# Kernel optimization log

Measured on AMD Instinct MI355X. Metric: run time of the kernel, lower is better.

## Reference

```python
import jax, jax.numpy as jnp
import numpy as np
import math

B, S, H = 1, 2048, 4096
NH, HD = 32, 128  # heads, head_dim
ROPE_THETA = 10000.0
SINK = 4
RECENT_RATIO = 0.1


def setup_inputs() -> dict:
    key = jax.random.key(0)
    ks = jax.random.split(key, 5)
    scale = 0.02
    return {
        "hidden_states": jax.random.normal(ks[0], (B, S, H), jnp.float32),
        "Wq": jax.random.normal(ks[1], (H, H), jnp.float32) * scale,
        "Wk": jax.random.normal(ks[2], (H, H), jnp.float32) * scale,
        "Wv": jax.random.normal(ks[3], (H, H), jnp.float32) * scale,
        "Wo": jax.random.normal(ks[4], (H, H), jnp.float32) * scale,
        "position_ids": jnp.arange(S, dtype=jnp.int64)[None, :],
    }


def _rope(x, cos, sin):
    # x: [B, NH, S, HD]; rotate_half = cat(-x2, x1)
    half = x.shape[-1] // 2
    rot = jnp.concatenate([-x[..., half:], x[..., :half]], axis=-1)
    return x * cos + rot * sin


def reference(hidden_states, Wq, Wk, Wv, Wo, position_ids):
    b, s, h = hidden_states.shape
    # projections (torch Linear: x @ W^T), split heads -> [B, NH, S, HD]
    q = (hidden_states @ Wq.T).reshape(b, s, NH, HD).transpose(0, 2, 1, 3)
    k = (hidden_states @ Wk.T).reshape(b, s, NH, HD).transpose(0, 2, 1, 3)
    v = (hidden_states @ Wv.T).reshape(b, s, NH, HD).transpose(0, 2, 1, 3)

    # rotary embeddings from position_ids
    inv_freq = 1.0 / (ROPE_THETA ** (jnp.arange(0, HD, 2, dtype=jnp.float32) / HD))
    freqs = position_ids.astype(jnp.float32)[..., None] * inv_freq  # [B, S, HD/2]
    emb = jnp.concatenate([freqs, freqs], axis=-1)                   # [B, S, HD]
    cos = jnp.cos(emb)[:, None, :, :]
    sin = jnp.sin(emb)[:, None, :, :]
    q = _rope(q, cos, sin)
    k = _rope(k, cos, sin)

    # causal attention
    scores = jnp.einsum('bhqd,bhkd->bhqk', q, k) / math.sqrt(HD)
    neg = jnp.finfo(scores.dtype).min
    causal = jnp.tril(jnp.ones((s, s), dtype=bool))
    scores = jnp.where(causal[None, None], scores, neg)
    attn = jax.nn.softmax(scores, axis=-1)
    out = jnp.einsum('bhqk,bhkd->bhqd', attn, v)
    out = out.transpose(0, 2, 1, 3).reshape(b, s, h)
    attn_output = out @ Wo.T

    # H2O streaming cache eviction: sink (first 4) + recent window KV
    recent = int(s * RECENT_RATIO)
    k_evicted = jnp.concatenate([k[:, :, :SINK, :], k[:, :, s - recent:, :]], axis=2)
    v_evicted = jnp.concatenate([v[:, :, :SINK, :], v[:, :, s - recent:, :]], axis=2)
    return attn_output, k_evicted, v_evicted
```

## Files before the change

### kernel.cpp

```cpp
#include <hip/hip_runtime.h>
#include <hip/hip_bf16.h>

typedef __bf16 bf16;
typedef __bf16 bf16x4 __attribute__((ext_vector_type(4)));
typedef __bf16 bf16x8 __attribute__((ext_vector_type(8)));
typedef float f32x4 __attribute__((ext_vector_type(4)));

#define MFMA16(a, b, c) __builtin_amdgcn_mfma_f32_16x16x32_bf16(a, b, c, 0, 0, 0)

constexpr int S_LEN = 2048;
constexpr int HDIM = 4096;
constexpr int NHEADS = 32;
constexpr int HEADD = 128;
constexpr int SINKN = 4;
constexpr int RECENT = 204;
constexpr int EVROWS = SINKN + RECENT;
constexpr float QSCALE = 0.08838834764831845f;

constexpr int JOBS_PER_HEAD = 40;
constexpr int SLOTS_PER_HEAD = 36;
constexpr size_t SLOT_BYTES = 33792;

__device__ inline bf16x8 cvt8(const float* p) {
    float4 a = *(const float4*)p;
    float4 b = *(const float4*)(p + 4);
    return bf16x8{(bf16)a.x, (bf16)a.y, (bf16)a.z, (bf16)a.w,
                  (bf16)b.x, (bf16)b.y, (bf16)b.z, (bf16)b.w};
}

__device__ inline void gload16(const bf16* g, bf16* l) {
    __builtin_amdgcn_global_load_lds(
        (const __attribute__((address_space(1))) unsigned int*)g,
        (__attribute__((address_space(3))) unsigned int*)l, 16, 0, 0);
}

__global__ __launch_bounds__(256) void cvt_kernel(const float* __restrict__ in,
                                                  bf16* __restrict__ out, int n8) {
    int i = blockIdx.x * 256 + threadIdx.x;
    if (i >= n8) return;
    *(bf16x8*)(out + (size_t)i * 8) = cvt8(in + (size_t)i * 8);
}

__device__ __forceinline__ void stage_b256(const bf16* __restrict__ Bp, bf16* dst,
                                           int K, int kc, int tid) {
#pragma unroll
    for (int r = 0; r < 2; ++r) {
        int idx = r * 512 + tid;
        int row = idx >> 3;
        int gs = (idx & 7) ^ (row & 7);
        gload16(Bp + (size_t)row * K + kc + gs * 8, dst + idx * 8);
    }
}
template <int MH>
__device__ __forceinline__ void stage_a256(const bf16* __restrict__ Ap, bf16* dst,
                                           int K, int kc, int tid) {
#pragma unroll
    for (int r = 0; r < 2; ++r) {
        int idx = r * 512 + tid;
        int row = idx >> 3;
        int gs = (idx & 7) ^ (row & 7);
        gload16(Ap + (size_t)(MH * 128 + row) * K + kc + gs * 8,
                dst + MH * 8192 + idx * 8);
    }
}
template <int MH>
__device__ __forceinline__ void lda256(const bf16* buf, int wm, int lg, int lr,
                                       bf16x8 (&af)[2][2]) {
#pragma unroll
    for (int mt = 0; mt < 2; ++mt)
#pragma unroll
        for (int kk = 0; kk < 2; ++kk)
            af[mt][kk] = *(const bf16x8*)&buf[MH * 8192 + (wm * 32 + mt * 16 + lr) * 64 +
                                              (((kk * 4 + lg) ^ (lr & 7)) * 8)];
}
__device__ __forceinline__ void ldb256(const bf16* buf, int wn, int lg, int lr,
                                       bf16x8 (&bfr)[4][2]) {
#pragma unroll
    for (int nt = 0; nt < 4; ++nt)
#pragma unroll
        for (int kk = 0; kk < 2; ++kk)
            bfr[nt][kk] = *(const bf16x8*)&buf[(wn * 64 + nt * 16 + lr) * 64 +
                                               (((kk * 4 + lg) ^ (lr & 7)) * 8)];
}
template <int MH>
__device__ __forceinline__ void mma256(const bf16x8 (&af)[2][2], const bf16x8 (&bfr)[4][2],
                                       f32x4 (&acc)[2][2][4]) {
#pragma unroll
    for (int mt = 0; mt < 2; ++mt)
#pragma unroll
        for (int nt = 0; nt < 4; ++nt)
#pragma unroll
            for (int kk = 0; kk < 2; ++kk)
                acc[MH][mt][nt] = MFMA16(af[mt][kk], bfr[nt][kk], acc[MH][mt][nt]);
}

template <bool C_IS_F32>
__global__ __launch_bounds__(512, 2) void gemm256(const bf16* __restrict__ A,
                                                  const bf16* __restrict__ B,
                                                  void* __restrict__ Cv,
                                                  int M, int N, int K) {
    __shared__ bf16 Abuf[2][256 * 64];
    __shared__ bf16 Bbuf[2][128 * 64];

    const int tid = threadIdx.x;
    const int lane = tid & 63, wid = tid >> 6;
    const int wm = wid >> 1, wn = wid & 1;
    const int lg = lane >> 4, lr = lane & 15;

    const int bid = blockIdx.x;
    const int bx = (bid & 7) * 4 + (bid >> 6);
    const int by = (bid >> 3) & 7;
    const int m0 = by * 256, n0 = bx * 128;

    const bf16* Ap = A + (size_t)m0 * K;
    const bf16* Bp = B + (size_t)n0 * K;

    f32x4 acc[2][2][4] = {};
    bf16x8 af[2][2], bfr[4][2];

    stage_b256(Bp, Bbuf[0], K, 0, tid);
    stage_a256<0>(Ap, Abuf[0], K, 0, tid);
    stage_a256<1>(Ap, Abuf[0], K, 0, tid);
    asm volatile("s_waitcnt vmcnt(2)" ::: "memory");
    __builtin_amdgcn_s_barrier();

    const bf16 *Ard = Abuf[0], *Brd = Bbuf[0];
    bf16 *Awr = Abuf[1], *Bwr = Bbuf[1];

    const int NT = K / 64;
    for (int t = 0; t < NT - 1; ++t) {
        const int kc = (t + 1) * 64;
        ldb256(Brd, wn, lg, lr, bfr);
        lda256<0>(Ard, wm, lg, lr, af);
        stage_b256(Bp, Bwr, K, kc, tid);
        stage_a256<0>(Ap, Awr, K, kc, tid);
        __builtin_amdgcn_s_barrier();
        asm volatile("s_waitcnt lgkmcnt(0)" ::: "memory");
        __builtin_amdgcn_sched_barrier(0);
        __builtin_amdgcn_s_setprio(1);
        mma256<0>(af, bfr, acc);
        __builtin_amdgcn_s_setprio(0);
        asm volatile("s_waitcnt vmcnt(4)" ::: "memory");
        __builtin_amdgcn_s_barrier();
        lda256<1>(Ard, wm, lg, lr, af);
        stage_a256<1>(Ap, Awr, K, kc, tid);
        __builtin_amdgcn_s_barrier();
        asm volatile("s_waitcnt lgkmcnt(0)" ::: "memory");
        __builtin_amdgcn_sched_barrier(0);
        __builtin_amdgcn_s_setprio(1);
        mma256<1>(af, bfr, acc);
        __builtin_amdgcn_s_setprio(0);
        asm volatile("s_waitcnt vmcnt(2)" ::: "memory");
        __builtin_amdgcn_s_barrier();
        const bf16* tA = Ard; Ard = Awr; Awr = (bf16*)tA;
        const bf16* tB = Brd; Brd = Bwr; Bwr = (bf16*)tB;
    }
    asm volatile("s_waitcnt vmcnt(0)" ::: "memory");
    __builtin_amdgcn_s_barrier();
    ldb256(Brd, wn, lg, lr, bfr);
    lda256<0>(Ard, wm, lg, lr, af);
    mma256<0>(af, bfr, acc);
    lda256<1>(Ard, wm, lg, lr, af);
    mma256<1>(af, bfr, acc);

#pragma unroll
    for (int mh = 0; mh < 2; ++mh)
#pragma unroll
        for (int mt = 0; mt < 2; ++mt)
#pragma unroll
            for (int nt = 0; nt < 4; ++nt)
#pragma unroll
                for (int r = 0; r < 4; ++r) {
                    int row = m0 + mh * 128 + wm * 32 + mt * 16 + lg * 4 + r;
                    int col = n0 + wn * 64 + nt * 16 + lr;
                    if constexpr (C_IS_F32)
                        ((float*)Cv)[(size_t)row * N + col] = acc[mh][mt][nt][r];
                    else
                        ((bf16*)Cv)[(size_t)row * N + col] = (bf16)acc[mh][mt][nt][r];
                }
}

__global__ __launch_bounds__(256) void rope_kernel(bf16* __restrict__ q,
                                                   bf16* __restrict__ k) {
    const int s = blockIdx.x;
    const int t = threadIdx.x;
    const int hh = t >> 3;
    const int i0 = (t & 7) << 3;
    const size_t base = (size_t)s * HDIM + hh * HEADD;

    bf16x8 q1 = *(bf16x8*)(q + base + i0);
    bf16x8 q2 = *(bf16x8*)(q + base + 64 + i0);
    bf16x8 k1 = *(bf16x8*)(k + base + i0);
    bf16x8 k2 = *(bf16x8*)(k + base + 64 + i0);
    bf16x8 q1o, q2o, k1o, k2o;
    const float pos = (float)s;
#pragma unroll
    for (int j = 0; j < 8; ++j) {
        float f = pos * exp2f((float)(i0 + j) * (-0.2076205059304602f));
        float sn, cs;
        sincosf(f, &sn, &cs);
        float x1 = (float)q1[j], x2 = (float)q2[j];
        q1o[j] = (bf16)((x1 * cs - x2 * sn) * QSCALE);
        q2o[j] = (bf16)((x2 * cs + x1 * sn) * QSCALE);
        x1 = (float)k1[j]; x2 = (float)k2[j];
        k1o[j] = (bf16)(x1 * cs - x2 * sn);
        k2o[j] = (bf16)(x2 * cs + x1 * sn);
    }
    *(bf16x8*)(q + base + i0) = q1o;
    *(bf16x8*)(q + base + 64 + i0) = q2o;
    *(bf16x8*)(k + base + i0) = k1o;
    *(bf16x8*)(k + base + 64 + i0) = k2o;
}

__global__ __launch_bounds__(256) void transpose_v(const bf16* __restrict__ v,
                                                   bf16* __restrict__ vt) {
    __shared__ bf16 tile[64][136];
    const int h = blockIdx.x;
    const int s0 = blockIdx.y * 64;
    const int tid = threadIdx.x;
#pragma unroll
    for (int j = 0; j < 4; ++j) {
        int ch = tid + 256 * j;
        int row = ch >> 4, c8 = (ch & 15) << 3;
        *(bf16x8*)&tile[row][c8] =
            *(const bf16x8*)(v + (size_t)(s0 + row) * HDIM + h * HEADD + c8);
    }
    __syncthreads();
#pragma unroll
    for (int j = 0; j < 4; ++j) {
        int ch = tid + 256 * j;
        int d = ch >> 3, s8 = (ch & 7) << 3;
        bf16x8 w;
#pragma unroll
        for (int i = 0; i < 8; ++i) w[i] = tile[s8 + i][d];
        *(bf16x8*)(vt + ((size_t)h * HEADD + d) * S_LEN + s0 + s8) = w;
    }
}

__global__ __launch_bounds__(256, 2) void attn_kernel(const bf16* __restrict__ q,
                                                      const bf16* __restrict__ k,
                                                      const bf16* __restrict__ vt,
                                                      bf16* __restrict__ o,
                                                      char* __restrict__ partials) {
    __shared__ bf16 K_lds[2][64 * 128];
    __shared__ bf16 V_lds[128 * 64];
    __shared__ bf16 P_lds[4][32 * 72];

    const int tid = threadIdx.x;
    const int lane = tid & 63, wid = tid >> 6;
    const int lg = lane >> 4, lr = lane & 15;

    const int bj = blockIdx.x;
    const int h = bj / JOBS_PER_HEAD;
    const int within = JOBS_PER_HEAD - 1 - (bj % JOBS_PER_HEAD);
    int qb, chunk, nj;
    if (within < 4)       { qb = within; chunk = 0; nj = 1; }
    else if (within < 12) { int u2 = within - 4;  qb = 4  + (u2 >> 1); chunk = u2 & 1;        nj = 2; }
    else if (within < 24) { int u2 = within - 12; int q3 = u2 / 3; qb = 8 + q3; chunk = u2 - 3 * q3; nj = 3; }
    else                  { int u2 = within - 24; qb = 12 + (u2 >> 2); chunk = u2 & 3;        nj = 4; }
    const int q0 = qb * 128;
    const int ntiles = 2 * qb + 2;
    const int tb = chunk * 8;
    const int te = min(tb + 8, ntiles);

    bf16x8 aq[2][4];
#pragma unroll
    for (int rs = 0; rs < 2; ++rs)
#pragma unroll
        for (int dc = 0; dc < 4; ++dc)
            aq[rs][dc] = *(const bf16x8*)(q + (size_t)(q0 + wid * 32 + rs * 16 + lr) * HDIM +
                                          h * HEADD + dc * 32 + lg * 8);

    f32x4 oacc[2][8] = {};
    float m_[2] = {-1e30f, -1e30f};
    float l_[2] = {0.f, 0.f};
    bf16* pw = &P_lds[wid][0];

    {
        const int kv0 = tb << 6;
#pragma unroll
        for (int i = 0; i < 4; ++i) {
            const int c = wid * 4 + i;
            const int krow = 4 * c + (lane >> 4);
            const int kg = (lane & 15) ^ (krow & 7);
            gload16(k + (size_t)(kv0 + krow) * HDIM + h * HEADD + kg * 8,
                    &K_lds[0][c * 512]);
        }
    }

    int cur = 0;
    for (int t = tb; t < te; ++t) {
        const int kv0 = t << 6;
#pragma unroll
        for (int i = 0; i < 4; ++i) {
            const int c = wid * 4 + i;
            const int vrow = 8 * c + (lane >> 3);
            const int vg = (lane & 7) ^ (vrow & 7);
            gload16(vt + (size_t)(h * HEADD + vrow) * S_LEN + kv0 + vg * 8,
                    &V_lds[c * 512]);
        }
        if (t + 1 < te) {
            const int kvn = (t + 1) << 6;
#pragma unroll
            for (int i = 0; i < 4; ++i) {
                const int c = wid * 4 + i;
                const int krow = 4 * c + (lane >> 4);
                const int kg = (lane & 15) ^ (krow & 7);
                gload16(k + (size_t)(kvn + krow) * HDIM + h * HEADD + kg * 8,
                        &K_lds[cur ^ 1][c * 512]);
            }
            asm volatile("s_waitcnt vmcnt(8)" ::: "memory");
        } else {
            asm volatile("s_waitcnt vmcnt(4)" ::: "memory");
        }
        __builtin_amdgcn_s_barrier();
        __builtin_amdgcn_sched_barrier(0);

        const bf16* Kb = &K_lds[cur][0];
        f32x4 st[2][4] = {};
#pragma unroll
        for (int kt = 0; kt < 4; ++kt) {
            bf16x8 kf[4];
#pragma unroll
            for (int dc = 0; dc < 4; ++dc)
                kf[dc] = *(const bf16x8*)&Kb[(kt * 16 + lr) * 128 +
                                             (((dc * 4 + lg) ^ (lr & 7)) * 8)];
#pragma unroll
            for (int dc = 0; dc < 4; ++dc) {
                st[0][kt] = MFMA16(kf[dc], aq[0][dc], st[0][kt]);
                st[1][kt] = MFMA16(kf[dc], aq[1][dc], st[1][kt]);
            }
        }

#pragma unroll
        for (int rs = 0; rs < 2; ++rs) {
            const int qr0 = q0 + wid * 32 + rs * 16;
            const int qidx = qr0 + lr;
            const bool nm = (kv0 + 63) > qr0;
            float v[16];
#pragma unroll
            for (int kt = 0; kt < 4; ++kt)
#pragma unroll
                for (int r = 0; r < 4; ++r) {
                    float x = st[rs][kt][r];
                    if (nm && (kv0 + kt * 16 + lg * 4 + r > qidx)) x = -1e30f;
                    v[kt * 4 + r] = x;
                }
            float pm = v[0];
#pragma unroll
            for (int i = 1; i < 16; ++i) pm = fmaxf(pm, v[i]);
            pm = fmaxf(pm, __shfl_xor(pm, 16));
            pm = fmaxf(pm, __shfl_xor(pm, 32));

            if (__any(pm > m_[rs] + 8.0f)) {
                float mn = fmaxf(m_[rs], pm);
                float sc = __expf(m_[rs] - mn);
                m_[rs] = mn;
                l_[rs] *= sc;
                float scb[4];
#pragma unroll
                for (int r = 0; r < 4; ++r)
                    scb[r] = __uint_as_float(__builtin_amdgcn_ds_bpermute(
                        (lg * 4 + r) * 4, __float_as_uint(sc)));
#pragma unroll
                for (int dt = 0; dt < 8; ++dt)
#pragma unroll
                    for (int r = 0; r < 4; ++r) oacc[rs][dt][r] *= scb[r];
            }
            const float mn = m_[rs];
            float rsum = 0.f;
#pragma unroll
            for (int kt = 0; kt < 4; ++kt) {
                bf16x4 pk;
#pragma unroll
                for (int r = 0; r < 4; ++r) {
                    float p = __expf(v[kt * 4 + r] - mn);
                    rsum += p;
                    pk[r] = (bf16)p;
                }
                *(bf16x4*)&pw[(rs * 16 + lr) * 72 + kt * 16 + lg * 4] = pk;
            }
            rsum += __shfl_xor(rsum, 16);
            rsum += __shfl_xor(rsum, 32);
            l_[rs] += rsum;
        }

        if (t + 1 < te) asm volatile("s_waitcnt vmcnt(4)" ::: "memory");
        else            asm volatile("s_waitcnt vmcnt(0)" ::: "memory");
        __builtin_amdgcn_s_barrier();
        __builtin_amdgcn_sched_barrier(0);

        bf16x8 pa[2][2];
#pragma unroll
        for (int rs = 0; rs < 2; ++rs)
#pragma unroll
            for (int kt2 = 0; kt2 < 2; ++kt2)
                pa[rs][kt2] = *(const bf16x8*)&pw[(rs * 16 + lr) * 72 + kt2 * 32 + lg * 8];
#pragma unroll
        for (int kt2 = 0; kt2 < 2; ++kt2)
#pragma unroll
            for (int dt = 0; dt < 8; ++dt) {
                bf16x8 bv = *(const bf16x8*)&V_lds[(dt * 16 + lr) * 64 +
                                                   (((kt2 * 4 + lg) ^ (lr & 7)) * 8)];
                oacc[0][dt] = MFMA16(pa[0][kt2], bv, oacc[0][dt]);
                oacc[1][dt] = MFMA16(pa[1][kt2], bv, oacc[1][dt]);
            }

        __builtin_amdgcn_s_barrier();
        __builtin_amdgcn_sched_barrier(0);
        cur ^= 1;
    }

    if (nj == 1) {
#pragma unroll
        for (int rs = 0; rs < 2; ++rs) {
            float lb[4];
#pragma unroll
            for (int r = 0; r < 4; ++r)
                lb[r] = __uint_as_float(__builtin_amdgcn_ds_bpermute(
                    (lg * 4 + r) * 4, __float_as_uint(l_[rs])));
#pragma unroll
            for (int r = 0; r < 4; ++r) {
                float inv = 1.0f / lb[r];
                const int row = q0 + wid * 32 + rs * 16 + lg * 4 + r;
#pragma unroll
                for (int dt = 0; dt < 8; ++dt)
                    o[(size_t)row * HDIM + h * HEADD + dt * 16 + lr] =
                        (bf16)(oacc[rs][dt][r] * inv);
            }
        }
    } else {
        const int sb = (qb < 8) ? (qb - 4) * 2 : (qb < 12) ? 8 + (qb - 8) * 3
                                                           : 20 + (qb - 12) * 4;
        char* slotp = partials + ((size_t)h * SLOTS_PER_HEAD + sb + chunk) * SLOT_BYTES;
        bf16* Op = (bf16*)slotp;
        float* mp = (float*)(slotp + 32768);
        float* lp = mp + 128;
#pragma unroll
        for (int rs = 0; rs < 2; ++rs) {
            const int rowl = wid * 32 + rs * 16;
#pragma unroll
            for (int r = 0; r < 4; ++r)
#pragma unroll
                for (int dt = 0; dt < 8; ++dt)
                    Op[(rowl + lg * 4 + r) * HEADD + dt * 16 + lr] = (bf16)oacc[rs][dt][r];
            if (lg == 0) { mp[rowl + lr] = m_[rs]; lp[rowl + lr] = l_[rs]; }
        }
    }
}

__global__ __launch_bounds__(256) void combine_kernel(const char* __restrict__ partials,
                                                      bf16* __restrict__ o) {
    const int h = blockIdx.x;
    const int qb = 4 + blockIdx.y;
    const int nj = (2 * qb + 9) / 8;
    const int sb = (qb < 8) ? (qb - 4) * 2 : (qb < 12) ? 8 + (qb - 8) * 3
                                                       : 20 + (qb - 12) * 4;
    const char* base = partials + ((size_t)h * SLOTS_PER_HEAD + sb) * SLOT_BYTES;

    const int row = threadIdx.x >> 1;
    const int d0 = (threadIdx.x & 1) * 64;

    float mc[4], lc[4];
    float M = -1e30f;
    for (int c = 0; c < nj; ++c) {
        const char* sp = base + (size_t)c * SLOT_BYTES;
        mc[c] = ((const float*)(sp + 32768))[row];
        lc[c] = ((const float*)(sp + 33280))[row];
        M = fmaxf(M, mc[c]);
    }
    float denom = 0.f;
    float acc[64] = {};
    for (int c = 0; c < nj; ++c) {
        float wgt = __expf(mc[c] - M);
        denom += wgt * lc[c];
        const bf16* Op = (const bf16*)(base + (size_t)c * SLOT_BYTES);
#pragma unroll
        for (int j = 0; j < 8; ++j) {
            bf16x8 a = *(const bf16x8*)&Op[row * HEADD + d0 + j * 8];
#pragma unroll
            for (int e = 0; e < 8; ++e) acc[j * 8 + e] += wgt * (float)a[e];
        }
    }
    float inv = 1.0f / denom;
    bf16* dst = o + (size_t)(qb * 128 + row) * HDIM + h * HEADD + d0;
#pragma unroll
    for (int j = 0; j < 8; ++j) {
        bf16x8 w;
#pragma unroll
        for (int e = 0; e < 8; ++e) w[e] = (bf16)(acc[j * 8 + e] * inv);
        *(bf16x8*)&dst[j * 8] = w;
    }
}

__global__ __launch_bounds__(256) void evict_kernel(const bf16* __restrict__ k,
                                                    const bf16* __restrict__ v,
                                                    float* __restrict__ out) {
    const int total = NHEADS * EVROWS * HEADD;
    int idx = blockIdx.x * 256 + threadIdx.x;
    if (idx >= 2 * total) return;
    const int which = idx / total;
    const int rem = idx % total;
    const int hh = rem / (EVROWS * HEADD);
    const int i = (rem / HEADD) % EVROWS;
    const int d = rem % HEADD;
    const int s = (i < SINKN) ? i : (S_LEN - RECENT) + (i - SINKN);
    const bf16* src = which ? v : k;
    out[(size_t)S_LEN * HDIM + (size_t)which * total + rem] =
        (float)src[(size_t)s * HDIM + hh * HEADD + d];
}

extern "C" void kernel_launch(void* const* d_in, const int* in_sizes, int n_in,
                              void* d_out, int out_size, void* d_ws, size_t ws_size,
                              hipStream_t stream) {
    const float* hs = (const float*)d_in[0];
    const float* Wq = (const float*)d_in[1];
    const float* Wk = (const float*)d_in[2];
    const float* Wv = (const float*)d_in[3];
    const float* Wo = (const float*)d_in[4];
    float* out = (float*)d_out;

    const size_t MB = 1024 * 1024;
    char* w = (char*)d_ws;
    bf16* hs_bf = (bf16*)(w);
    bf16* W_bf  = (bf16*)(w + 16 * MB);
    char* part  = w;
    bf16* q_ws  = (bf16*)(w + 48 * MB);
    bf16* k_ws  = (bf16*)(w + 64 * MB);
    bf16* v_ws  = (bf16*)(w + 80 * MB);
    bf16* vt_ws = (bf16*)(w + 96 * MB);
    bf16* o_ws  = q_ws;

    const int nW8 = HDIM * HDIM / 8;
    const int nH8 = S_LEN * HDIM / 8;

    cvt_kernel<<<(nH8 + 255) / 256, 256, 0, stream>>>(hs, hs_bf, nH8);

    cvt_kernel<<<(nW8 + 255) / 256, 256, 0, stream>>>(Wq, W_bf, nW8);
    gemm256<false><<<256, 512, 0, stream>>>(hs_bf, W_bf, q_ws, S_LEN, HDIM, HDIM);
    cvt_kernel<<<(nW8 + 255) / 256, 256, 0, stream>>>(Wk, W_bf, nW8);
    gemm256<false><<<256, 512, 0, stream>>>(hs_bf, W_bf, k_ws, S_LEN, HDIM, HDIM);
    cvt_kernel<<<(nW8 + 255) / 256, 256, 0, stream>>>(Wv, W_bf, nW8);
    gemm256<false><<<256, 512, 0, stream>>>(hs_bf, W_bf, v_ws, S_LEN, HDIM, HDIM);

    rope_kernel<<<S_LEN, 256, 0, stream>>>(q_ws, k_ws);
    transpose_v<<<dim3(NHEADS, S_LEN / 64), 256, 0, stream>>>(v_ws, vt_ws);

    evict_kernel<<<(2 * NHEADS * EVROWS * HEADD + 255) / 256, 256, 0, stream>>>(k_ws, v_ws, out);

    attn_kernel<<<NHEADS * JOBS_PER_HEAD, 256, 0, stream>>>(q_ws, k_ws, vt_ws, o_ws, part);
    combine_kernel<<<dim3(NHEADS, 12), 256, 0, stream>>>(part, o_ws);

    cvt_kernel<<<(nW8 + 255) / 256, 256, 0, stream>>>(Wo, W_bf, nW8);
    gemm256<true><<<256, 512, 0, stream>>>(o_ws, W_bf, out, S_LEN, HDIM, HDIM);
}
```

Before: 443.5 us.

## Fuse fp32-to-bf16 weight conversion into GEMM B-operand staging

Removes the four standalone weight conversion kernels and has each GEMM load fp32 weight tiles into registers, convert them to bf16, and write them into swizzled LDS itself. This avoids writing and re-reading a 32MB bf16 copy of each weight matrix and saves four launches. In exchange, B tiles now pass through registers instead of direct global-to-LDS loads, each block reads twice the bytes for B, and the pipeline's waitcnt and barrier placement changes, which may expose more load latency.

```diff
diff --git a/kernel.cpp b/kernel.cpp
--- a/kernel.cpp
+++ b/kernel.cpp
@@ -28,6 +28,11 @@
                   (bf16)b.x, (bf16)b.y, (bf16)b.z, (bf16)b.w};
 }
 
+__device__ __forceinline__ bf16x8 cvt8f(const float4& a, const float4& b) {
+    return bf16x8{(bf16)a.x, (bf16)a.y, (bf16)a.z, (bf16)a.w,
+                  (bf16)b.x, (bf16)b.y, (bf16)b.z, (bf16)b.w};
+}
+
 __device__ inline void gload16(const bf16* g, bf16* l) {
     __builtin_amdgcn_global_load_lds(
         (const __attribute__((address_space(1))) unsigned int*)g,
@@ -41,16 +46,6 @@
     *(bf16x8*)(out + (size_t)i * 8) = cvt8(in + (size_t)i * 8);
 }
 
-__device__ __forceinline__ void stage_b256(const bf16* __restrict__ Bp, bf16* dst,
-                                           int K, int kc, int tid) {
-#pragma unroll
-    for (int r = 0; r < 2; ++r) {
-        int idx = r * 512 + tid;
-        int row = idx >> 3;
-        int gs = (idx & 7) ^ (row & 7);
-        gload16(Bp + (size_t)row * K + kc + gs * 8, dst + idx * 8);
-    }
-}
 template <int MH>
 __device__ __forceinline__ void stage_a256(const bf16* __restrict__ Ap, bf16* dst,
                                            int K, int kc, int tid) {
@@ -63,6 +58,20 @@
                 dst + MH * 8192 + idx * 8);
     }
 }
+__device__ __forceinline__ void loadB_f32(const float* __restrict__ Bp, int K, int kc,
+                                          int tid, float4 (&br)[4]) {
+    const float* p = Bp + (size_t)(tid >> 2) * K + kc + (tid & 3) * 16;
+    br[0] = *(const float4*)p;
+    br[1] = *(const float4*)(p + 4);
+    br[2] = *(const float4*)(p + 8);
+    br[3] = *(const float4*)(p + 12);
+}
+__device__ __forceinline__ void writeB_lds(bf16* dst, int tid, const float4 (&br)[4]) {
+    const int row = tid >> 2;
+    const int c8 = (tid & 3) * 2;
+    *(bf16x8*)&dst[row * 64 + ((c8 ^ (row & 7)) * 8)] = cvt8f(br[0], br[1]);
+    *(bf16x8*)&dst[row * 64 + (((c8 + 1) ^ (row & 7)) * 8)] = cvt8f(br[2], br[3]);
+}
 template <int MH>
 __device__ __forceinline__ void lda256(const bf16* buf, int wm, int lg, int lr,
                                        bf16x8 (&af)[2][2]) {
@@ -96,7 +105,7 @@
 
 template <bool C_IS_F32>
 __global__ __launch_bounds__(512, 2) void gemm256(const bf16* __restrict__ A,
-                                                  const bf16* __restrict__ B,
+                                                  const float* __restrict__ B,
                                                   void* __restrict__ Cv,
                                                   int M, int N, int K) {
     __shared__ bf16 Abuf[2][256 * 64];
@@ -113,15 +122,20 @@
     const int m0 = by * 256, n0 = bx * 128;
 
     const bf16* Ap = A + (size_t)m0 * K;
-    const bf16* Bp = B + (size_t)n0 * K;
+    const float* Bp = B + (size_t)n0 * K;
 
     f32x4 acc[2][2][4] = {};
     bf16x8 af[2][2], bfr[4][2];
-
-    stage_b256(Bp, Bbuf[0], K, 0, tid);
+    float4 br[4];
+
+    loadB_f32(Bp, K, 0, tid, br);
+    __builtin_amdgcn_sched_barrier(0);
     stage_a256<0>(Ap, Abuf[0], K, 0, tid);
     stage_a256<1>(Ap, Abuf[0], K, 0, tid);
-    asm volatile("s_waitcnt vmcnt(2)" ::: "memory");
+    __builtin_amdgcn_sched_barrier(0);
+    asm volatile("s_waitcnt vmcnt(4)" ::: "memory");
+    writeB_lds(Bbuf[0], tid, br);
+    asm volatile("s_waitcnt vmcnt(0) lgkmcnt(0)" ::: "memory");
     __builtin_amdgcn_s_barrier();
 
     const bf16 *Ard = Abuf[0], *Brd = Bbuf[0];
@@ -132,7 +146,8 @@
         const int kc = (t + 1) * 64;
         ldb256(Brd, wn, lg, lr, bfr);
         lda256<0>(Ard, wm, lg, lr, af);
-        stage_b256(Bp, Bwr, K, kc, tid);
+        loadB_f32(Bp, K, kc, tid, br);
+        __builtin_amdgcn_sched_barrier(0);
         stage_a256<0>(Ap, Awr, K, kc, tid);
         __builtin_amdgcn_s_barrier();
         asm volatile("s_waitcnt lgkmcnt(0)" ::: "memory");
@@ -140,27 +155,29 @@
         __builtin_amdgcn_s_setprio(1);
         mma256<0>(af, bfr, acc);
         __builtin_amdgcn_s_setprio(0);
-        asm volatile("s_waitcnt vmcnt(4)" ::: "memory");
-        __builtin_amdgcn_s_barrier();
         lda256<1>(Ard, wm, lg, lr, af);
         stage_a256<1>(Ap, Awr, K, kc, tid);
-        __builtin_amdgcn_s_barrier();
+        __builtin_amdgcn_sched_barrier(0);
+        asm volatile("s_waitcnt vmcnt(4)" ::: "memory");
+        writeB_lds(Bwr, tid, br);
         asm volatile("s_waitcnt lgkmcnt(0)" ::: "memory");
         __builtin_amdgcn_sched_barrier(0);
         __builtin_amdgcn_s_setprio(1);
         mma256<1>(af, bfr, acc);
         __builtin_amdgcn_s_setprio(0);
-        asm volatile("s_waitcnt vmcnt(2)" ::: "memory");
+        asm volatile("s_waitcnt vmcnt(0)" ::: "memory");
         __builtin_amdgcn_s_barrier();
         const bf16* tA = Ard; Ard = Awr; Awr = (bf16*)tA;
         const bf16* tB = Brd; Brd = Bwr; Bwr = (bf16*)tB;
     }
-    asm volatile("s_waitcnt vmcnt(0)" ::: "memory");
-    __builtin_amdgcn_s_barrier();
     ldb256(Brd, wn, lg, lr, bfr);
     lda256<0>(Ard, wm, lg, lr, af);
+    asm volatile("s_waitcnt lgkmcnt(0)" ::: "memory");
+    __builtin_amdgcn_sched_barrier(0);
     mma256<0>(af, bfr, acc);
     lda256<1>(Ard, wm, lg, lr, af);
+    asm volatile("s_waitcnt lgkmcnt(0)" ::: "memory");
+    __builtin_amdgcn_sched_barrier(0);
     mma256<1>(af, bfr, acc);
 
 #pragma unroll
@@ -523,7 +540,6 @@
     const size_t MB = 1024 * 1024;
     char* w = (char*)d_ws;
     bf16* hs_bf = (bf16*)(w);
-    bf16* W_bf  = (bf16*)(w + 16 * MB);
     char* part  = w;
     bf16* q_ws  = (bf16*)(w + 48 * MB);
     bf16* k_ws  = (bf16*)(w + 64 * MB);
@@ -531,17 +547,13 @@
     bf16* vt_ws = (bf16*)(w + 96 * MB);
     bf16* o_ws  = q_ws;
 
-    const int nW8 = HDIM * HDIM / 8;
     const int nH8 = S_LEN * HDIM / 8;
 
     cvt_kernel<<<(nH8 + 255) / 256, 256, 0, stream>>>(hs, hs_bf, nH8);
 
-    cvt_kernel<<<(nW8 + 255) / 256, 256, 0, stream>>>(Wq, W_bf, nW8);
-    gemm256<false><<<256, 512, 0, stream>>>(hs_bf, W_bf, q_ws, S_LEN, HDIM, HDIM);
-    cvt_kernel<<<(nW8 + 255) / 256, 256, 0, stream>>>(Wk, W_bf, nW8);
-    gemm256<false><<<256, 512, 0, stream>>>(hs_bf, W_bf, k_ws, S_LEN, HDIM, HDIM);
-    cvt_kernel<<<(nW8 + 255) / 256, 256, 0, stream>>>(Wv, W_bf, nW8);
-    gemm256<false><<<256, 512, 0, stream>>>(hs_bf, W_bf, v_ws, S_LEN, HDIM, HDIM);
+    gemm256<false><<<256, 512, 0, stream>>>(hs_bf, Wq, q_ws, S_LEN, HDIM, HDIM);
+    gemm256<false><<<256, 512, 0, stream>>>(hs_bf, Wk, k_ws, S_LEN, HDIM, HDIM);
+    gemm256<false><<<256, 512, 0, stream>>>(hs_bf, Wv, v_ws, S_LEN, HDIM, HDIM);
 
     rope_kernel<<<S_LEN, 256, 0, stream>>>(q_ws, k_ws);
     transpose_v<<<dim3(NHEADS, S_LEN / 64), 256, 0, stream>>>(v_ws, vt_ws);
@@ -551,6 +563,5 @@
     attn_kernel<<<NHEADS * JOBS_PER_HEAD, 256, 0, stream>>>(q_ws, k_ws, vt_ws, o_ws, part);
     combine_kernel<<<dim3(NHEADS, 12), 256, 0, stream>>>(part, o_ws);
 
-    cvt_kernel<<<(nW8 + 255) / 256, 256, 0, stream>>>(Wo, W_bf, nW8);
-    gemm256<true><<<256, 512, 0, stream>>>(o_ws, W_bf, out, S_LEN, HDIM, HDIM);
-}
+    gemm256<true><<<256, 512, 0, stream>>>(o_ws, Wo, out, S_LEN, HDIM, HDIM);
+}
```

Result: slower. 639.3 us (+44.1%).

## Shrink projection GEMM tiles to 128x128 and simplify the double-buffer pipeline

Applied to the files above, without the earlier changes.

The projection GEMMs now use 128x128 output tiles instead of 256x128 and launch 512 blocks instead of 256. Launch bounds are raised to allow 4 blocks per CU with half the A-tile shared memory. The split two-half MFMA pipeline becomes a simpler loop: stage the next tile, wait, then load fragments and compute. This aims to fill more CUs and raise occupancy, at the cost of less data reuse per tile and more global/L2 traffic.

```diff
diff --git a/kernel.cpp b/kernel.cpp
--- a/kernel.cpp
+++ b/kernel.cpp
@@ -41,39 +41,35 @@
     *(bf16x8*)(out + (size_t)i * 8) = cvt8(in + (size_t)i * 8);
 }
 
-__device__ __forceinline__ void stage_b256(const bf16* __restrict__ Bp, bf16* dst,
-                                           int K, int kc, int tid) {
+__device__ __forceinline__ void stage128(const bf16* __restrict__ Ap,
+                                         const bf16* __restrict__ Bp,
+                                         bf16* Adst, bf16* Bdst,
+                                         int K, int kc, int tid) {
 #pragma unroll
     for (int r = 0; r < 2; ++r) {
         int idx = r * 512 + tid;
         int row = idx >> 3;
         int gs = (idx & 7) ^ (row & 7);
-        gload16(Bp + (size_t)row * K + kc + gs * 8, dst + idx * 8);
-    }
-}
-template <int MH>
-__device__ __forceinline__ void stage_a256(const bf16* __restrict__ Ap, bf16* dst,
-                                           int K, int kc, int tid) {
+        gload16(Ap + (size_t)row * K + kc + gs * 8, Adst + idx * 8);
+    }
 #pragma unroll
     for (int r = 0; r < 2; ++r) {
         int idx = r * 512 + tid;
         int row = idx >> 3;
         int gs = (idx & 7) ^ (row & 7);
-        gload16(Ap + (size_t)(MH * 128 + row) * K + kc + gs * 8,
-                dst + MH * 8192 + idx * 8);
-    }
-}
-template <int MH>
-__device__ __forceinline__ void lda256(const bf16* buf, int wm, int lg, int lr,
+        gload16(Bp + (size_t)row * K + kc + gs * 8, Bdst + idx * 8);
+    }
+}
+__device__ __forceinline__ void lda128(const bf16* buf, int wm, int lg, int lr,
                                        bf16x8 (&af)[2][2]) {
 #pragma unroll
     for (int mt = 0; mt < 2; ++mt)
 #pragma unroll
         for (int kk = 0; kk < 2; ++kk)
-            af[mt][kk] = *(const bf16x8*)&buf[MH * 8192 + (wm * 32 + mt * 16 + lr) * 64 +
+            af[mt][kk] = *(const bf16x8*)&buf[(wm * 32 + mt * 16 + lr) * 64 +
                                               (((kk * 4 + lg) ^ (lr & 7)) * 8)];
 }
-__device__ __forceinline__ void ldb256(const bf16* buf, int wn, int lg, int lr,
+__device__ __forceinline__ void ldb128(const bf16* buf, int wn, int lg, int lr,
                                        bf16x8 (&bfr)[4][2]) {
 #pragma unroll
     for (int nt = 0; nt < 4; ++nt)
@@ -82,24 +78,13 @@
             bfr[nt][kk] = *(const bf16x8*)&buf[(wn * 64 + nt * 16 + lr) * 64 +
                                                (((kk * 4 + lg) ^ (lr & 7)) * 8)];
 }
-template <int MH>
-__device__ __forceinline__ void mma256(const bf16x8 (&af)[2][2], const bf16x8 (&bfr)[4][2],
-                                       f32x4 (&acc)[2][2][4]) {
-#pragma unroll
-    for (int mt = 0; mt < 2; ++mt)
-#pragma unroll
-        for (int nt = 0; nt < 4; ++nt)
-#pragma unroll
-            for (int kk = 0; kk < 2; ++kk)
-                acc[MH][mt][nt] = MFMA16(af[mt][kk], bfr[nt][kk], acc[MH][mt][nt]);
-}
 
 template <bool C_IS_F32>
-__global__ __launch_bounds__(512, 2) void gemm256(const bf16* __restrict__ A,
+__global__ __launch_bounds__(512, 4) void gemm128(const bf16* __restrict__ A,
                                                   const bf16* __restrict__ B,
                                                   void* __restrict__ Cv,
                                                   int M, int N, int K) {
-    __shared__ bf16 Abuf[2][256 * 64];
+    __shared__ bf16 Abuf[2][128 * 64];
     __shared__ bf16 Bbuf[2][128 * 64];
 
     const int tid = threadIdx.x;
@@ -108,76 +93,70 @@
     const int lg = lane >> 4, lr = lane & 15;
 
     const int bid = blockIdx.x;
-    const int bx = (bid & 7) * 4 + (bid >> 6);
-    const int by = (bid >> 3) & 7;
-    const int m0 = by * 256, n0 = bx * 128;
+    const int xcd = bid & 7, wi = bid >> 3;
+    const int bx = xcd * 4 + (wi >> 4);
+    const int by = wi & 15;
+    const int m0 = by * 128, n0 = bx * 128;
 
     const bf16* Ap = A + (size_t)m0 * K;
     const bf16* Bp = B + (size_t)n0 * K;
 
-    f32x4 acc[2][2][4] = {};
+    f32x4 acc[2][4] = {};
     bf16x8 af[2][2], bfr[4][2];
 
-    stage_b256(Bp, Bbuf[0], K, 0, tid);
-    stage_a256<0>(Ap, Abuf[0], K, 0, tid);
-    stage_a256<1>(Ap, Abuf[0], K, 0, tid);
-    asm volatile("s_waitcnt vmcnt(2)" ::: "memory");
-    __builtin_amdgcn_s_barrier();
-
-    const bf16 *Ard = Abuf[0], *Brd = Bbuf[0];
-    bf16 *Awr = Abuf[1], *Bwr = Bbuf[1];
-
+    stage128(Ap, Bp, Abuf[0], Bbuf[0], K, 0, tid);
+
+    int cur = 0;
     const int NT = K / 64;
     for (int t = 0; t < NT - 1; ++t) {
-        const int kc = (t + 1) * 64;
-        ldb256(Brd, wn, lg, lr, bfr);
-        lda256<0>(Ard, wm, lg, lr, af);
-        stage_b256(Bp, Bwr, K, kc, tid);
-        stage_a256<0>(Ap, Awr, K, kc, tid);
+        stage128(Ap, Bp, Abuf[cur ^ 1], Bbuf[cur ^ 1], K, (t + 1) * 64, tid);
+        asm volatile("s_waitcnt vmcnt(4)" ::: "memory");
         __builtin_amdgcn_s_barrier();
+        __builtin_amdgcn_sched_barrier(0);
+
+        lda128(Abuf[cur], wm, lg, lr, af);
+        ldb128(Bbuf[cur], wn, lg, lr, bfr);
         asm volatile("s_waitcnt lgkmcnt(0)" ::: "memory");
         __builtin_amdgcn_sched_barrier(0);
         __builtin_amdgcn_s_setprio(1);
-        mma256<0>(af, bfr, acc);
+#pragma unroll
+        for (int mt = 0; mt < 2; ++mt)
+#pragma unroll
+            for (int nt = 0; nt < 4; ++nt)
+#pragma unroll
+                for (int kk = 0; kk < 2; ++kk)
+                    acc[mt][nt] = MFMA16(af[mt][kk], bfr[nt][kk], acc[mt][nt]);
         __builtin_amdgcn_s_setprio(0);
-        asm volatile("s_waitcnt vmcnt(4)" ::: "memory");
         __builtin_amdgcn_s_barrier();
-        lda256<1>(Ard, wm, lg, lr, af);
-        stage_a256<1>(Ap, Awr, K, kc, tid);
-        __builtin_amdgcn_s_barrier();
-        asm volatile("s_waitcnt lgkmcnt(0)" ::: "memory");
-        __builtin_amdgcn_sched_barrier(0);
-        __builtin_amdgcn_s_setprio(1);
-        mma256<1>(af, bfr, acc);
-        __builtin_amdgcn_s_setprio(0);
-        asm volatile("s_waitcnt vmcnt(2)" ::: "memory");
-        __builtin_amdgcn_s_barrier();
-        const bf16* tA = Ard; Ard = Awr; Awr = (bf16*)tA;
-        const bf16* tB = Brd; Brd = Bwr; Bwr = (bf16*)tB;
+        cur ^= 1;
     }
     asm volatile("s_waitcnt vmcnt(0)" ::: "memory");
     __builtin_amdgcn_s_barrier();
-    ldb256(Brd, wn, lg, lr, bfr);
-    lda256<0>(Ard, wm, lg, lr, af);
-    mma256<0>(af, bfr, acc);
-    lda256<1>(Ard, wm, lg, lr, af);
-    mma256<1>(af, bfr, acc);
-
-#pragma unroll
-    for (int mh = 0; mh < 2; ++mh)
-#pragma unroll
-        for (int mt = 0; mt < 2; ++mt)
-#pragma unroll
-            for (int nt = 0; nt < 4; ++nt)
-#pragma unroll
-                for (int r = 0; r < 4; ++r) {
-                    int row = m0 + mh * 128 + wm * 32 + mt * 16 + lg * 4 + r;
-                    int col = n0 + wn * 64 + nt * 16 + lr;
-                    if constexpr (C_IS_F32)
-                        ((float*)Cv)[(size_t)row * N + col] = acc[mh][mt][nt][r];
-                    else
-                        ((bf16*)Cv)[(size_t)row * N + col] = (bf16)acc[mh][mt][nt][r];
-                }
+    lda128(Abuf[cur], wm, lg, lr, af);
+    ldb128(Bbuf[cur], wn, lg, lr, bfr);
+    asm volatile("s_waitcnt lgkmcnt(0)" ::: "memory");
+    __builtin_amdgcn_sched_barrier(0);
+#pragma unroll
+    for (int mt = 0; mt < 2; ++mt)
+#pragma unroll
+        for (int nt = 0; nt < 4; ++nt)
+#pragma unroll
+            for (int kk = 0; kk < 2; ++kk)
+                acc[mt][nt] = MFMA16(af[mt][kk], bfr[nt][kk], acc[mt][nt]);
+
+#pragma unroll
+    for (int mt = 0; mt < 2; ++mt)
+#pragma unroll
+        for (int nt = 0; nt < 4; ++nt)
+#pragma unroll
+            for (int r = 0; r < 4; ++r) {
+                int row = m0 + wm * 32 + mt * 16 + lg * 4 + r;
+                int col = n0 + wn * 64 + nt * 16 + lr;
+                if constexpr (C_IS_F32)
+                    ((float*)Cv)[(size_t)row * N + col] = acc[mt][nt][r];
+                else
+                    ((bf16*)Cv)[(size_t)row * N + col] = (bf16)acc[mt][nt][r];
+            }
 }
 
 __global__ __launch_bounds__(256) void rope_kernel(bf16* __restrict__ q,
@@ -537,11 +516,11 @@
     cvt_kernel<<<(nH8 + 255) / 256, 256, 0, stream>>>(hs, hs_bf, nH8);
 
     cvt_kernel<<<(nW8 + 255) / 256, 256, 0, stream>>>(Wq, W_bf, nW8);
-    gemm256<false><<<256, 512, 0, stream>>>(hs_bf, W_bf, q_ws, S_LEN, HDIM, HDIM);
+    gemm128<false><<<512, 512, 0, stream>>>(hs_bf, W_bf, q_ws, S_LEN, HDIM, HDIM);
     cvt_kernel<<<(nW8 + 255) / 256, 256, 0, stream>>>(Wk, W_bf, nW8);
-    gemm256<false><<<256, 512, 0, stream>>>(hs_bf, W_bf, k_ws, S_LEN, HDIM, HDIM);
+    gemm128<false><<<512, 512, 0, stream>>>(hs_bf, W_bf, k_ws, S_LEN, HDIM, HDIM);
     cvt_kernel<<<(nW8 + 255) / 256, 256, 0, stream>>>(Wv, W_bf, nW8);
-    gemm256<false><<<256, 512, 0, stream>>>(hs_bf, W_bf, v_ws, S_LEN, HDIM, HDIM);
+    gemm128<false><<<512, 512, 0, stream>>>(hs_bf, W_bf, v_ws, S_LEN, HDIM, HDIM);
 
     rope_kernel<<<S_LEN, 256, 0, stream>>>(q_ws, k_ws);
     transpose_v<<<dim3(NHEADS, S_LEN / 64), 256, 0, stream>>>(v_ws, vt_ws);
@@ -552,5 +531,5 @@
     combine_kernel<<<dim3(NHEADS, 12), 256, 0, stream>>>(part, o_ws);
 
     cvt_kernel<<<(nW8 + 255) / 256, 256, 0, stream>>>(Wo, W_bf, nW8);
-    gemm256<true><<<256, 512, 0, stream>>>(o_ws, W_bf, out, S_LEN, HDIM, HDIM);
-}
+    gemm128<true><<<512, 512, 0, stream>>>(o_ws, W_bf, out, S_LEN, HDIM, HDIM);
+}
```

New measurement: 455.4 us. 2.7% more time.
